# Performance work log

Measured on AMD Instinct MI355X. Metric: run time of the kernel, lower is better.

## Reference

```python
import jax, jax.numpy as jnp
import numpy as np

N_NODES = 250000
N_EDGES = 4000000
N_GRAPHS = 512
NEG_SLOPE = 0.01  # F.leaky_relu default


def _glorot(key, shape):
    fan_in, fan_out = shape
    lim = (6.0 / (fan_in + fan_out)) ** 0.5
    return jax.random.uniform(key, shape, jnp.float32, -lim, lim)


def setup_inputs() -> dict:
    key = jax.random.key(0)
    ks = jax.random.split(key, 12)
    x = jax.random.normal(ks[0], (N_NODES, 13), jnp.float32)
    edge_index = jax.random.randint(ks[1], (2, N_EDGES), 0, N_NODES, jnp.int64)
    batch_index = jnp.sort(jax.random.randint(ks[2], (N_NODES,), 0, N_GRAPHS, jnp.int64))
    # SAGEConv params: lin_l (neighbor agg, with bias), lin_r (self, no bias)
    dims = [(13, 16), (16, 8), (8, 4)]
    params = {}
    for i, (di, do) in enumerate(dims, 1):
        params[f'W{i}l'] = _glorot(ks[2 + 2 * i], (di, do))
        params[f'b{i}'] = jnp.zeros((do,), jnp.float32)
        params[f'W{i}r'] = _glorot(ks[3 + 2 * i], (di, do))
    params['Wc'] = _glorot(ks[10], (8, 1))
    params['bc'] = jnp.zeros((1,), jnp.float32)
    return dict(x=x, edge_index=edge_index, batch_index=batch_index, **params)


def _sage_conv(x, src, dst, Wl, bl, Wr):
    # mean-aggregate neighbor features at target nodes, then linear
    msg_sum = jax.ops.segment_sum(x[src], dst, num_segments=N_NODES)  # [N, d]
    cnt = jax.ops.segment_sum(jnp.ones((src.shape[0],), x.dtype), dst,
                              num_segments=N_NODES)
    agg = msg_sum / jnp.maximum(cnt, 1.0)[:, None]
    return agg @ Wl + bl + x @ Wr


def reference(x, edge_index, batch_index,
              W1l, b1, W1r, W2l, b2, W2r, W3l, b3, W3r, Wc, bc):
    src, dst = edge_index[0], edge_index[1]
    h = jax.nn.leaky_relu(_sage_conv(x, src, dst, W1l, b1, W1r), NEG_SLOPE)
    h = jax.nn.leaky_relu(_sage_conv(h, src, dst, W2l, b2, W2r), NEG_SLOPE)
    h = _sage_conv(h, src, dst, W3l, b3, W3r)  # [N, 4]
    add_pool = jax.ops.segment_sum(h, batch_index, num_segments=N_GRAPHS)  # [G,4]
    gcnt = jax.ops.segment_sum(jnp.ones((N_NODES,), h.dtype), batch_index,
                               num_segments=N_GRAPHS)
    mean_pool = add_pool / jnp.maximum(gcnt, 1.0)[:, None]
    g = jnp.concatenate([mean_pool, add_pool], axis=1)  # [G, 8]
    return g @ Wc + bc  # [G, 1]
```

## Files before the change

### kernel.cpp

```cpp
#include <hip/hip_runtime.h>

#define N_NODES 250000
#define N_EDGES 4000000
#define N_GRAPHS 512
#define NEG 0.01f
#define BINB 9
#define WIN 512
#define NBINS 489
#define NSUB (NBINS * 4)
#define CAPQ 2560
#define PART_EPB 8192
#define PART_BLOCKS 489

__device__ __forceinline__ float lrelu(float v) { return v > 0.0f ? v : NEG * v; }
__device__ __forceinline__ unsigned f2b(float f) {
    unsigned u = __float_as_uint(f);
    unsigned r = ((u >> 16) & 1u) + 0x7FFFu;
    return (u + r) >> 16;
}
__device__ __forceinline__ unsigned pk(float a, float b) { return f2b(a) | (f2b(b) << 16); }
__device__ __forceinline__ float blo(unsigned p) { return __uint_as_float(p << 16); }
__device__ __forceinline__ float bhi(unsigned p) { return __uint_as_float(p & 0xFFFF0000u); }

__global__ void pack_x(const float* __restrict__ x, unsigned* __restrict__ x16b,
                       int* __restrict__ qcnt) {
    if (blockIdx.x == 0) {
        for (int i = threadIdx.x; i < NSUB; i += 256) qcnt[i] = 0;
    }
    int tid = blockIdx.x * blockDim.x + threadIdx.x;
    if (tid >= N_NODES * 8) return;
    int n = tid >> 3, d2 = tid & 7;
    int a = d2 * 2, b = a + 1;
    float va = (a < 13) ? x[n * 13 + a] : 0.0f;
    float vb = (b < 13) ? x[n * 13 + b] : 0.0f;
    x16b[tid] = pk(va, vb);
}

__global__ __launch_bounds__(1024) void partition_k(const int* __restrict__ src,
                                                    const int* __restrict__ dst,
                                                    int* __restrict__ qcnt,
                                                    unsigned* __restrict__ binned) {
    __shared__ int hist[NSUB];
    __shared__ int base[NSUB];
    int t = threadIdx.x;
    for (int i = t; i < NSUB; i += 1024) hist[i] = 0;
    __syncthreads();
    unsigned e0 = blockIdx.x * PART_EPB;
    for (int i = 0; i < PART_EPB / 1024; i++) {
        unsigned e = e0 + (unsigned)i * 1024u + t;
        if (e < N_EDGES) {
            int s = ((dst[e] >> BINB) << 2) | (src[e] >> 16);
            atomicAdd(&hist[s], 1);
        }
    }
    __syncthreads();
    for (int i = t; i < NSUB; i += 1024) {
        int h = hist[i];
        base[i] = (h > 0) ? atomicAdd(&qcnt[i], h) : 0;
        hist[i] = 0;
    }
    __syncthreads();
    for (int i = 0; i < PART_EPB / 1024; i++) {
        unsigned e = e0 + (unsigned)i * 1024u + t;
        if (e < N_EDGES) {
            int d = dst[e], sv = src[e];
            int s = ((d >> BINB) << 2) | (sv >> 16);
            int pos = base[s] + atomicAdd(&hist[s], 1);
            binned[(size_t)s * CAPQ + pos] =
                ((unsigned)(d & (WIN - 1)) << 18) | (unsigned)sv;
        }
    }
}

__global__ __launch_bounds__(1024) void sortagg_k(const unsigned* __restrict__ x16b,
                                                  unsigned* __restrict__ binned,
                                                  const int* __restrict__ qcnt,
                                                  int* __restrict__ offs,
                                                  float* __restrict__ cntf,
                                                  float* __restrict__ agg) {
    __shared__ unsigned stg[CAPQ];
    __shared__ unsigned srt[CAPQ];
    __shared__ int hist[WIN];
    __shared__ int cur[WIN];
    __shared__ int wsum[8];
    int t = threadIdx.x;
    int bin = blockIdx.x;
    int f = t & (WIN - 1), l = t >> 9;
    int lane = t & 63, wv = t >> 6;
    float a0 = 0, a1 = 0, a2 = 0, a3 = 0, a4 = 0, a5 = 0, a6 = 0, a7 = 0;
    int deg = 0;
    for (int q = 0; q < 4; q++) {
        int sub = (bin << 2) | q;
        int cnt = qcnt[sub];
        unsigned* bp = binned + (size_t)sub * CAPQ;
        if (t < WIN) hist[t] = 0;
        __syncthreads();
        for (int i = t; i < cnt; i += 1024) {
            unsigned w = bp[i];
            stg[i] = w;
            atomicAdd(&hist[w >> 18], 1);
        }
        __syncthreads();
        int v = (t < WIN) ? hist[t] : 0;
#pragma unroll
        for (int d = 1; d < 64; d <<= 1) {
            int u = __shfl_up(v, d, 64);
            if (lane >= d) v += u;
        }
        if (t < WIN && lane == 63) wsum[wv] = v;
        __syncthreads();
        if (t == 0) {
            int r = 0;
#pragma unroll
            for (int i = 0; i < 8; i++) { int s = wsum[i]; wsum[i] = r; r += s; }
        }
        __syncthreads();
        if (t < WIN) {
            int incl = v + wsum[wv];
            int ex = incl - hist[t];
            cur[t] = ex;
            offs[(size_t)sub * 513 + t] = ex;
            deg += hist[t];
        }
        if (t == 0) offs[(size_t)sub * 513 + WIN] = cnt;
        __syncthreads();
        for (int i = t; i < cnt; i += 1024) {
            unsigned w = stg[i];
            int pos = atomicAdd(&cur[w >> 18], 1);
            srt[pos] = w;
        }
        __syncthreads();
        for (int i = t; i < cnt; i += 1024) bp[i] = srt[i];
        int e_ = cur[f];
        int s_ = e_ - hist[f];
        int k = s_;
        for (; k + 4 <= e_; k += 4) {
            unsigned w0 = srt[k], w1 = srt[k + 1], w2 = srt[k + 2], w3 = srt[k + 3];
            uint4 v0 = *(const uint4*)&x16b[(size_t)(w0 & 0x3FFFFu) * 8u + (unsigned)(l * 4)];
            uint4 v1 = *(const uint4*)&x16b[(size_t)(w1 & 0x3FFFFu) * 8u + (unsigned)(l * 4)];
            uint4 v2 = *(const uint4*)&x16b[(size_t)(w2 & 0x3FFFFu) * 8u + (unsigned)(l * 4)];
            uint4 v3 = *(const uint4*)&x16b[(size_t)(w3 & 0x3FFFFu) * 8u + (unsigned)(l * 4)];
            a0 += blo(v0.x) + blo(v1.x) + blo(v2.x) + blo(v3.x);
            a1 += bhi(v0.x) + bhi(v1.x) + bhi(v2.x) + bhi(v3.x);
            a2 += blo(v0.y) + blo(v1.y) + blo(v2.y) + blo(v3.y);
            a3 += bhi(v0.y) + bhi(v1.y) + bhi(v2.y) + bhi(v3.y);
            a4 += blo(v0.z) + blo(v1.z) + blo(v2.z) + blo(v3.z);
            a5 += bhi(v0.z) + bhi(v1.z) + bhi(v2.z) + bhi(v3.z);
            a6 += blo(v0.w) + blo(v1.w) + blo(v2.w) + blo(v3.w);
            a7 += bhi(v0.w) + bhi(v1.w) + bhi(v2.w) + bhi(v3.w);
        }
        for (; k < e_; k++) {
            unsigned w = srt[k];
            uint4 v4 = *(const uint4*)&x16b[(size_t)(w & 0x3FFFFu) * 8u + (unsigned)(l * 4)];
            a0 += blo(v4.x); a1 += bhi(v4.x); a2 += blo(v4.y); a3 += bhi(v4.y);
            a4 += blo(v4.z); a5 += bhi(v4.z); a6 += blo(v4.w); a7 += bhi(v4.w);
        }
        __syncthreads();
    }
    int g = (bin << BINB) + f;
    if (g < N_NODES) {
        size_t b = (size_t)g * 13;
        if (l == 0) {
            agg[b + 0] = a0; agg[b + 1] = a1; agg[b + 2] = a2; agg[b + 3] = a3;
            agg[b + 4] = a4; agg[b + 5] = a5; agg[b + 6] = a6; agg[b + 7] = a7;
            cntf[g] = (float)deg;
        } else {
            agg[b + 8] = a0; agg[b + 9] = a1; agg[b + 10] = a2;
            agg[b + 11] = a3; agg[b + 12] = a4;
        }
    }
}

__global__ void fused1(const float* __restrict__ agg, const float* __restrict__ x,
                       const float* __restrict__ cntf,
                       const float* __restrict__ W1l, const float* __restrict__ b1,
                       const float* __restrict__ W1r, const float* __restrict__ W2l,
                       const float* __restrict__ W2r,
                       unsigned* __restrict__ y2b, float* __restrict__ z2) {
    __shared__ float sWl[208], sWr[208], sb[16], sA[128], sB[128];
    for (int i = threadIdx.x; i < 208; i += blockDim.x) { sWl[i] = W1l[i]; sWr[i] = W1r[i]; }
    for (int i = threadIdx.x; i < 128; i += blockDim.x) { sA[i] = W2l[i]; sB[i] = W2r[i]; }
    if (threadIdx.x < 16) sb[threadIdx.x] = b1[threadIdx.x];
    __syncthreads();
    int n = blockIdx.x * blockDim.x + threadIdx.x;
    if (n >= N_NODES) return;
    float inv = 1.0f / fmaxf(cntf[n], 1.0f);
    float a[13], xv[13];
#pragma unroll
    for (int i = 0; i < 13; i++) { a[i] = agg[n * 13 + i] * inv; xv[i] = x[n * 13 + i]; }
    float h[16];
#pragma unroll
    for (int o = 0; o < 16; o++) {
        float acc = sb[o];
#pragma unroll
        for (int i = 0; i < 13; i++) acc += a[i] * sWl[i * 16 + o] + xv[i] * sWr[i * 16 + o];
        h[o] = lrelu(acc);
    }
    float ya[8];
#pragma unroll
    for (int o2 = 0; o2 < 8; o2++) {
        float y = 0.0f, za = 0.0f;
#pragma unroll
        for (int o = 0; o < 16; o++) { y += h[o] * sA[o * 8 + o2]; za += h[o] * sB[o * 8 + o2]; }
        ya[o2] = y;
        z2[n * 8 + o2] = za;
    }
    uint4 out;
    out.x = pk(ya[0], ya[1]); out.y = pk(ya[2], ya[3]);
    out.z = pk(ya[4], ya[5]); out.w = pk(ya[6], ya[7]);
    *(uint4*)&y2b[(size_t)n * 4u] = out;
}

__global__ __launch_bounds__(256) void agg8f_k(const unsigned* __restrict__ y2b,
                                               const unsigned* __restrict__ binned,
                                               const int* __restrict__ offs,
                                               const float* __restrict__ cntf,
                                               const float* __restrict__ b2,
                                               const float* __restrict__ W3l,
                                               float* __restrict__ z2h2,
                                               unsigned* __restrict__ y3b,
                                               float* __restrict__ pool) {
    __shared__ float sb[8], sW3[32];
    if (blockIdx.x == 0) {
        for (int i = threadIdx.x; i < N_GRAPHS * 5; i += 256) pool[i] = 0.0f;
    }
    if (threadIdx.x < 8) sb[threadIdx.x] = b2[threadIdx.x];
    if (threadIdx.x < 32) sW3[threadIdx.x] = W3l[threadIdx.x];
    __syncthreads();
    int g = blockIdx.x * 256 + threadIdx.x;
    if (g >= N_NODES) return;
    int bin = g >> BINB, f = g & (WIN - 1);
    float a0 = 0, a1 = 0, a2 = 0, a3 = 0, a4 = 0, a5 = 0, a6 = 0, a7 = 0;
#pragma unroll
    for (int q = 0; q < 4; q++) {
        int sub = (bin << 2) | q;
        const int* o = offs + (size_t)sub * 513;
        int s = o[f], e = o[f + 1];
        const unsigned* bp = binned + (size_t)sub * CAPQ;
        int k = s;
        for (; k + 4 <= e; k += 4) {
            unsigned w0 = bp[k], w1 = bp[k + 1], w2 = bp[k + 2], w3 = bp[k + 3];
            uint4 v0 = *(const uint4*)&y2b[(size_t)(w0 & 0x3FFFFu) * 4u];
            uint4 v1 = *(const uint4*)&y2b[(size_t)(w1 & 0x3FFFFu) * 4u];
            uint4 v2 = *(const uint4*)&y2b[(size_t)(w2 & 0x3FFFFu) * 4u];
            uint4 v3 = *(const uint4*)&y2b[(size_t)(w3 & 0x3FFFFu) * 4u];
            a0 += blo(v0.x) + blo(v1.x) + blo(v2.x) + blo(v3.x);
            a1 += bhi(v0.x) + bhi(v1.x) + bhi(v2.x) + bhi(v3.x);
            a2 += blo(v0.y) + blo(v1.y) + blo(v2.y) + blo(v3.y);
            a3 += bhi(v0.y) + bhi(v1.y) + bhi(v2.y) + bhi(v3.y);
            a4 += blo(v0.z) + blo(v1.z) + blo(v2.z) + blo(v3.z);
            a5 += bhi(v0.z) + bhi(v1.z) + bhi(v2.z) + bhi(v3.z);
            a6 += blo(v0.w) + blo(v1.w) + blo(v2.w) + blo(v3.w);
            a7 += bhi(v0.w) + bhi(v1.w) + bhi(v2.w) + bhi(v3.w);
        }
        for (; k < e; k++) {
            uint4 v = *(const uint4*)&y2b[(size_t)(bp[k] & 0x3FFFFu) * 4u];
            a0 += blo(v.x); a1 += bhi(v.x); a2 += blo(v.y); a3 += bhi(v.y);
            a4 += blo(v.z); a5 += bhi(v.z); a6 += blo(v.w); a7 += bhi(v.w);
        }
    }
    float inv = 1.0f / fmaxf(cntf[g], 1.0f);
    float h2v[8];
    float s8[8] = {a0, a1, a2, a3, a4, a5, a6, a7};
#pragma unroll
    for (int j = 0; j < 8; j++) {
        float v = s8[j] * inv + sb[j] + z2h2[(size_t)g * 8 + j];
        h2v[j] = lrelu(v);
        z2h2[(size_t)g * 8 + j] = h2v[j];
    }
    float y[4];
#pragma unroll
    for (int k = 0; k < 4; k++) {
        float acc = 0.0f;
#pragma unroll
        for (int j = 0; j < 8; j++) acc += h2v[j] * sW3[j * 4 + k];
        y[k] = acc;
    }
    uint2 out;
    out.x = pk(y[0], y[1]); out.y = pk(y[2], y[3]);
    *(uint2*)&y3b[(size_t)g * 2u] = out;
}

__global__ __launch_bounds__(256) void agg4pool_k(const unsigned* __restrict__ y3b,
                                                  const unsigned* __restrict__ binned,
                                                  const int* __restrict__ offs,
                                                  const float* __restrict__ cntf,
                                                  const float* __restrict__ h2,
                                                  const float* __restrict__ W3r,
                                                  const float* __restrict__ b3,
                                                  const int* __restrict__ batch,
                                                  float* __restrict__ pool,
                                                  float* __restrict__ gcnt) {
    __shared__ float sW[32], sb[4];
    __shared__ float lp[16][4];
    __shared__ float lc[16];
    __shared__ int sbase;
    if (threadIdx.x < 32) sW[threadIdx.x] = W3r[threadIdx.x];
    if (threadIdx.x < 4) sb[threadIdx.x] = b3[threadIdx.x];
    if (threadIdx.x < 16) {
        lc[threadIdx.x] = 0.0f;
        for (int k = 0; k < 4; k++) lp[threadIdx.x][k] = 0.0f;
    }
    int n0 = blockIdx.x * 256;
    if (threadIdx.x == 0) sbase = batch[n0 < N_NODES ? n0 : N_NODES - 1];
    __syncthreads();
    int g = n0 + threadIdx.x;
    if (g < N_NODES) {
        int bin = g >> BINB, f = g & (WIN - 1);
        float a0 = 0, a1 = 0, a2 = 0, a3 = 0;
#pragma unroll
        for (int q = 0; q < 4; q++) {
            int sub = (bin << 2) | q;
            const int* o = offs + (size_t)sub * 513;
            int s = o[f], e = o[f + 1];
            const unsigned* bp = binned + (size_t)sub * CAPQ;
            int k = s;
            for (; k + 4 <= e; k += 4) {
                unsigned w0 = bp[k], w1 = bp[k + 1], w2 = bp[k + 2], w3 = bp[k + 3];
                uint2 v0 = *(const uint2*)&y3b[(size_t)(w0 & 0x3FFFFu) * 2u];
                uint2 v1 = *(const uint2*)&y3b[(size_t)(w1 & 0x3FFFFu) * 2u];
                uint2 v2 = *(const uint2*)&y3b[(size_t)(w2 & 0x3FFFFu) * 2u];
                uint2 v3 = *(const uint2*)&y3b[(size_t)(w3 & 0x3FFFFu) * 2u];
                a0 += blo(v0.x) + blo(v1.x) + blo(v2.x) + blo(v3.x);
                a1 += bhi(v0.x) + bhi(v1.x) + bhi(v2.x) + bhi(v3.x);
                a2 += blo(v0.y) + blo(v1.y) + blo(v2.y) + blo(v3.y);
                a3 += bhi(v0.y) + bhi(v1.y) + bhi(v2.y) + bhi(v3.y);
            }
            for (; k < e; k++) {
                uint2 v = *(const uint2*)&y3b[(size_t)(bp[k] & 0x3FFFFu) * 2u];
                a0 += blo(v.x); a1 += bhi(v.x); a2 += blo(v.y); a3 += bhi(v.y);
            }
        }
        float inv = 1.0f / fmaxf(cntf[g], 1.0f);
        float s4[4] = {a0, a1, a2, a3};
        float h2v[8];
#pragma unroll
        for (int j = 0; j < 8; j++) h2v[j] = h2[(size_t)g * 8 + j];
        int b = batch[g];
        int off = b - sbase;
        bool local = (off >= 0 && off < 16);
#pragma unroll
        for (int k = 0; k < 4; k++) {
            float z = 0.0f;
#pragma unroll
            for (int j = 0; j < 8; j++) z += h2v[j] * sW[j * 4 + k];
            float v = s4[k] * inv + sb[k] + z;
            if (local) atomicAdd(&lp[off][k], v);
            else atomicAdd(&pool[b * 4 + k], v);
        }
        if (local) atomicAdd(&lc[off], 1.0f);
        else atomicAdd(&gcnt[b], 1.0f);
    }
    __syncthreads();
    if (threadIdx.x < 16) {
        int b = sbase + threadIdx.x;
        float c = lc[threadIdx.x];
        if (c > 0.0f && b < N_GRAPHS) {
            atomicAdd(&gcnt[b], c);
            for (int k = 0; k < 4; k++) atomicAdd(&pool[b * 4 + k], lp[threadIdx.x][k]);
        }
    }
}

__global__ void final_k(const float* __restrict__ pool, const float* __restrict__ gcnt,
                        const float* __restrict__ Wc, const float* __restrict__ bc,
                        float* __restrict__ out) {
    int g = blockIdx.x * blockDim.x + threadIdx.x;
    if (g >= N_GRAPHS) return;
    float inv = 1.0f / fmaxf(gcnt[g], 1.0f);
    float acc = bc[0];
#pragma unroll
    for (int k = 0; k < 4; k++) {
        float ap = pool[g * 4 + k];
        acc += ap * inv * Wc[k] + ap * Wc[4 + k];
    }
    out[g] = acc;
}

extern "C" void kernel_launch(void* const* d_in, const int* in_sizes, int n_in,
                              void* d_out, int out_size, void* d_ws, size_t ws_size,
                              hipStream_t stream) {
    const float* x = (const float*)d_in[0];
    const int* ei = (const int*)d_in[1];
    const int* src = ei;
    const int* dst = ei + N_EDGES;
    const int* batch = (const int*)d_in[2];
    const float* W1l = (const float*)d_in[3];
    const float* b1 = (const float*)d_in[4];
    const float* W1r = (const float*)d_in[5];
    const float* W2l = (const float*)d_in[6];
    const float* b2 = (const float*)d_in[7];
    const float* W2r = (const float*)d_in[8];
    const float* W3l = (const float*)d_in[9];
    const float* b3 = (const float*)d_in[10];
    const float* W3r = (const float*)d_in[11];
    const float* Wc = (const float*)d_in[12];
    const float* bc = (const float*)d_in[13];
    float* out = (float*)d_out;

    const size_t N = N_NODES;
    unsigned* binned = (unsigned*)d_ws;
    int* qcnt = (int*)(binned + (size_t)NSUB * CAPQ);
    int* offs = qcnt + 2048;
    float* fbase = (float*)(offs + (size_t)NSUB * 513);
    float* agg = fbase;
    float* cntf = fbase + 13 * N;
    float* z2 = cntf + N;
    unsigned* x16b = (unsigned*)(z2 + 8 * N);
    unsigned* y2b = x16b + 8 * N;
    unsigned* y3b = y2b + 4 * N;
    float* pool = (float*)(y3b + 2 * N);
    float* gcnt = pool + N_GRAPHS * 4;

    const int TPB = 256;
    const int NB = (N_NODES + TPB - 1) / TPB;

    pack_x<<<(N_NODES * 8 + TPB - 1) / TPB, TPB, 0, stream>>>(x, x16b, qcnt);
    partition_k<<<PART_BLOCKS, 1024, 0, stream>>>(src, dst, qcnt, binned);
    sortagg_k<<<NBINS, 1024, 0, stream>>>(x16b, binned, qcnt, offs, cntf, agg);
    fused1<<<NB, TPB, 0, stream>>>(agg, x, cntf, W1l, b1, W1r, W2l, W2r, y2b, z2);
    agg8f_k<<<NB, TPB, 0, stream>>>(y2b, binned, offs, cntf, b2, W3l, z2, y3b, pool);
    agg4pool_k<<<NB, TPB, 0, stream>>>(y3b, binned, offs, cntf, z2, W3r, b3, batch, pool, gcnt);
    final_k<<<2, TPB, 0, stream>>>(pool, gcnt, Wc, bc, out);
}
```

Measured before the change: 318.4 us.

## Fuse layer-1 dense transform into sortagg and coalesce partition scatter via LDS

The layer-1 linear, leaky-relu and layer-2 projection (formerly the separate fused1 kernel) now run at the end of sortagg_k, reading the aggregated sums from LDS instead of writing and re-reading a 13-float agg buffer. Self features now come from the packed bf16 x16b instead of the fp32 x. partition_k now computes local prefix offsets and stages edges sorted by sub-bin in LDS before writing, so global writes to binned are contiguous runs. The changes remove a kernel launch and a global round trip and make the scatter writes more coalesced. The cost is more LDS per block (possibly lower occupancy), and the self term is now computed from bf16-rounded x.

```diff
diff --git a/kernel.cpp b/kernel.cpp
--- a/kernel.cpp
+++ b/kernel.cpp
@@ -41,34 +41,63 @@
                                                     int* __restrict__ qcnt,
                                                     unsigned* __restrict__ binned) {
     __shared__ int hist[NSUB];
+    __shared__ int loff[NSUB];
     __shared__ int base[NSUB];
+    __shared__ unsigned ebuf[PART_EPB];
+    __shared__ unsigned short subid[PART_EPB];
+    __shared__ int wsum[16];
     int t = threadIdx.x;
     for (int i = t; i < NSUB; i += 1024) hist[i] = 0;
     __syncthreads();
     unsigned e0 = blockIdx.x * PART_EPB;
-    for (int i = 0; i < PART_EPB / 1024; i++) {
-        unsigned e = e0 + (unsigned)i * 1024u + t;
-        if (e < N_EDGES) {
-            int s = ((dst[e] >> BINB) << 2) | (src[e] >> 16);
-            atomicAdd(&hist[s], 1);
-        }
+    int m = min((int)PART_EPB, (int)(N_EDGES - e0));
+    for (int i = t; i < m; i += 1024) {
+        unsigned e = e0 + i;
+        int s = ((dst[e] >> BINB) << 2) | (src[e] >> 16);
+        atomicAdd(&hist[s], 1);
+    }
+    __syncthreads();
+    int p = 0, s0 = 0, incl = 0;
+    if (t < NSUB / 2) { s0 = hist[2 * t]; p = s0 + hist[2 * t + 1]; }
+    incl = p;
+#pragma unroll
+    for (int d = 1; d < 64; d <<= 1) {
+        int u = __shfl_up(incl, d, 64);
+        if ((t & 63) >= d) incl += u;
+    }
+    if ((t & 63) == 63) wsum[t >> 6] = incl;
+    __syncthreads();
+    if (t == 0) {
+        int r = 0;
+#pragma unroll
+        for (int i = 0; i < 16; i++) { int s = wsum[i]; wsum[i] = r; r += s; }
+    }
+    __syncthreads();
+    if (t < NSUB / 2) {
+        int ex = incl + wsum[t >> 6] - p;
+        loff[2 * t] = ex;
+        loff[2 * t + 1] = ex + s0;
     }
     __syncthreads();
     for (int i = t; i < NSUB; i += 1024) {
         int h = hist[i];
         base[i] = (h > 0) ? atomicAdd(&qcnt[i], h) : 0;
-        hist[i] = 0;
-    }
-    __syncthreads();
-    for (int i = 0; i < PART_EPB / 1024; i++) {
-        unsigned e = e0 + (unsigned)i * 1024u + t;
-        if (e < N_EDGES) {
-            int d = dst[e], sv = src[e];
-            int s = ((d >> BINB) << 2) | (sv >> 16);
-            int pos = base[s] + atomicAdd(&hist[s], 1);
-            binned[(size_t)s * CAPQ + pos] =
-                ((unsigned)(d & (WIN - 1)) << 18) | (unsigned)sv;
-        }
+    }
+    __syncthreads();
+    for (int i = t; i < NSUB; i += 1024) hist[i] = loff[i];
+    __syncthreads();
+    for (int i = t; i < m; i += 1024) {
+        unsigned e = e0 + i;
+        int d = dst[e], sv = src[e];
+        int s = ((d >> BINB) << 2) | (sv >> 16);
+        int pos = atomicAdd(&hist[s], 1);
+        ebuf[pos] = ((unsigned)(d & (WIN - 1)) << 18) | (unsigned)sv;
+        subid[pos] = (unsigned short)s;
+    }
+    __syncthreads();
+    for (int j = t; j < m; j += 1024) {
+        int s = subid[j];
+        binned[(size_t)s * CAPQ + base[s] + (j - loff[s])] = ebuf[j];
     }
 }
 
@@ -77,12 +106,21 @@
                                                   const int* __restrict__ qcnt,
                                                   int* __restrict__ offs,
                                                   float* __restrict__ cntf,
-                                                  float* __restrict__ agg) {
-    __shared__ unsigned stg[CAPQ];
-    __shared__ unsigned srt[CAPQ];
-    __shared__ int hist[WIN];
-    __shared__ int cur[WIN];
-    __shared__ int wsum[8];
+                                                  const float* __restrict__ W1l,
+                                                  const float* __restrict__ b1,
+                                                  const float* __restrict__ W1r,
+                                                  const float* __restrict__ W2l,
+                                                  const float* __restrict__ W2r,
+                                                  unsigned* __restrict__ y2b,
+                                                  float* __restrict__ z2) {
+    __shared__ __align__(16) unsigned char sm[35584];
+    unsigned* stg = (unsigned*)sm;
+    unsigned* srt = stg + CAPQ;
+    int* hist = (int*)(srt + CAPQ);
+    int* cur = hist + WIN;
+    int* wsum = cur + WIN;
+    float* sagg = (float*)sm;
+    float* swt = sagg + 8192;
     int t = threadIdx.x;
     int bin = blockIdx.x;
     int f = t & (WIN - 1), l = t >> 9;
@@ -157,58 +195,64 @@
         }
         __syncthreads();
     }
-    int g = (bin << BINB) + f;
-    if (g < N_NODES) {
-        size_t b = (size_t)g * 13;
-        if (l == 0) {
-            agg[b + 0] = a0; agg[b + 1] = a1; agg[b + 2] = a2; agg[b + 3] = a3;
-            agg[b + 4] = a4; agg[b + 5] = a5; agg[b + 6] = a6; agg[b + 7] = a7;
+    {
+        float av[8] = {a0, a1, a2, a3, a4, a5, a6, a7};
+#pragma unroll
+        for (int i = 0; i < 8; i++) sagg[(f << 4) + (l << 3) + i] = av[i];
+    }
+    for (int i = t; i < 688; i += 1024) {
+        float w;
+        if (i < 208) w = W1l[i];
+        else if (i < 416) w = W1r[i - 208];
+        else if (i < 432) w = b1[i - 416];
+        else if (i < 560) w = W2l[i - 432];
+        else w = W2r[i - 560];
+        swt[i] = w;
+    }
+    __syncthreads();
+    if (t < WIN) {
+        int g = (bin << BINB) + t;
+        if (g < N_NODES) {
+            const float* sWl = swt;
+            const float* sWr = swt + 208;
+            const float* sbb = swt + 416;
+            const float* sA = swt + 432;
+            const float* sB = swt + 560;
+            float inv = 1.0f / (float)max(deg, 1);
+            float a[13], xv[13];
+#pragma unroll
+            for (int i = 0; i < 13; i++) a[i] = sagg[(t << 4) + i] * inv;
+#pragma unroll
+            for (int i2 = 0; i2 < 7; i2++) {
+                unsigned u = x16b[(size_t)g * 8 + i2];
+                xv[2 * i2] = blo(u);
+                if (2 * i2 + 1 < 13) xv[2 * i2 + 1] = bhi(u);
+            }
+            float h[16];
+#pragma unroll
+            for (int o = 0; o < 16; o++) {
+                float acc = sbb[o];
+#pragma unroll
+                for (int i = 0; i < 13; i++) acc += a[i] * sWl[i * 16 + o] + xv[i] * sWr[i * 16 + o];
+                h[o] = lrelu(acc);
+            }
+            float ya[8], z[8];
+#pragma unroll
+            for (int o2 = 0; o2 < 8; o2++) {
+                float y = 0.0f, za = 0.0f;
+#pragma unroll
+                for (int o = 0; o < 16; o++) { y += h[o] * sA[o * 8 + o2]; za += h[o] * sB[o * 8 + o2]; }
+                ya[o2] = y; z[o2] = za;
+            }
+            uint4 o4;
+            o4.x = pk(ya[0], ya[1]); o4.y = pk(ya[2], ya[3]);
+            o4.z = pk(ya[4], ya[5]); o4.w = pk(ya[6], ya[7]);
+            *(uint4*)&y2b[(size_t)g * 4u] = o4;
+            *(float4*)&z2[(size_t)g * 8] = make_float4(z[0], z[1], z[2], z[3]);
+            *(float4*)&z2[(size_t)g * 8 + 4] = make_float4(z[4], z[5], z[6], z[7]);
             cntf[g] = (float)deg;
-        } else {
-            agg[b + 8] = a0; agg[b + 9] = a1; agg[b + 10] = a2;
-            agg[b + 11] = a3; agg[b + 12] = a4;
-        }
-    }
-}
-
-__global__ void fused1(const float* __restrict__ agg, const float* __restrict__ x,
-                       const float* __restrict__ cntf,
-                       const float* __restrict__ W1l, const float* __restrict__ b1,
-                       const float* __restrict__ W1r, const float* __restrict__ W2l,
-                       const float* __restrict__ W2r,
-                       unsigned* __restrict__ y2b, float* __restrict__ z2) {
-    __shared__ float sWl[208], sWr[208], sb[16], sA[128], sB[128];
-    for (int i = threadIdx.x; i < 208; i += blockDim.x) { sWl[i] = W1l[i]; sWr[i] = W1r[i]; }
-    for (int i = threadIdx.x; i < 128; i += blockDim.x) { sA[i] = W2l[i]; sB[i] = W2r[i]; }
-    if (threadIdx.x < 16) sb[threadIdx.x] = b1[threadIdx.x];
-    __syncthreads();
-    int n = blockIdx.x * blockDim.x + threadIdx.x;
-    if (n >= N_NODES) return;
-    float inv = 1.0f / fmaxf(cntf[n], 1.0f);
-    float a[13], xv[13];
-#pragma unroll
-    for (int i = 0; i < 13; i++) { a[i] = agg[n * 13 + i] * inv; xv[i] = x[n * 13 + i]; }
-    float h[16];
-#pragma unroll
-    for (int o = 0; o < 16; o++) {
-        float acc = sb[o];
-#pragma unroll
-        for (int i = 0; i < 13; i++) acc += a[i] * sWl[i * 16 + o] + xv[i] * sWr[i * 16 + o];
-        h[o] = lrelu(acc);
-    }
-    float ya[8];
-#pragma unroll
-    for (int o2 = 0; o2 < 8; o2++) {
-        float y = 0.0f, za = 0.0f;
-#pragma unroll
-        for (int o = 0; o < 16; o++) { y += h[o] * sA[o * 8 + o2]; za += h[o] * sB[o * 8 + o2]; }
-        ya[o2] = y;
-        z2[n * 8 + o2] = za;
-    }
-    uint4 out;
-    out.x = pk(ya[0], ya[1]); out.y = pk(ya[2], ya[3]);
-    out.z = pk(ya[4], ya[5]); out.w = pk(ya[6], ya[7]);
-    *(uint4*)&y2b[(size_t)n * 4u] = out;
+        }
+    }
 }
 
 __global__ __launch_bounds__(256) void agg8f_k(const unsigned* __restrict__ y2b,
@@ -403,8 +447,7 @@
     int* qcnt = (int*)(binned + (size_t)NSUB * CAPQ);
     int* offs = qcnt + 2048;
     float* fbase = (float*)(offs + (size_t)NSUB * 513);
-    float* agg = fbase;
-    float* cntf = fbase + 13 * N;
+    float* cntf = fbase;
     float* z2 = cntf + N;
     unsigned* x16b = (unsigned*)(z2 + 8 * N);
     unsigned* y2b = x16b + 8 * N;
@@ -417,8 +460,8 @@
 
     pack_x<<<(N_NODES * 8 + TPB - 1) / TPB, TPB, 0, stream>>>(x, x16b, qcnt);
     partition_k<<<PART_BLOCKS, 1024, 0, stream>>>(src, dst, qcnt, binned);
-    sortagg_k<<<NBINS, 1024, 0, stream>>>(x16b, binned, qcnt, offs, cntf, agg);
-    fused1<<<NB, TPB, 0, stream>>>(agg, x, cntf, W1l, b1, W1r, W2l, W2r, y2b, z2);
+    sortagg_k<<<NBINS, 1024, 0, stream>>>(x16b, binned, qcnt, offs, cntf,
+                                          W1l, b1, W1r, W2l, W2r, y2b, z2);
     agg8f_k<<<NB, TPB, 0, stream>>>(y2b, binned, offs, cntf, b2, W3l, z2, y3b, pool);
     agg4pool_k<<<NB, TPB, 0, stream>>>(y3b, binned, offs, cntf, z2, W3r, b3, batch, pool, gcnt);
     final_k<<<2, TPB, 0, stream>>>(pool, gcnt, Wc, bc, out);
```

After: 355.0 us. 11.5% more time.

## Stage partitioned edges in shared memory for coalesced bucket writes

Applied to the files above, without the earlier changes.

The partition kernel now computes a block-local exclusive prefix over sub-bin histograms and scatters each edge into a shared-memory buffer ordered by sub-bin. It then writes the buffer out sequentially, so consecutive threads write contiguous runs within each global bucket instead of scattering randomly. This aims to cut uncoalesced global stores. In exchange it uses roughly 60KB of LDS, which lowers occupancy, and adds extra scan and synchronisation steps.

```diff
diff --git a/kernel.cpp b/kernel.cpp
--- a/kernel.cpp
+++ b/kernel.cpp
@@ -41,34 +41,63 @@
                                                     int* __restrict__ qcnt,
                                                     unsigned* __restrict__ binned) {
     __shared__ int hist[NSUB];
+    __shared__ int loff[NSUB];
     __shared__ int base[NSUB];
+    __shared__ unsigned ebuf[PART_EPB];
+    __shared__ unsigned short subid[PART_EPB];
+    __shared__ int wsum[16];
     int t = threadIdx.x;
     for (int i = t; i < NSUB; i += 1024) hist[i] = 0;
     __syncthreads();
     unsigned e0 = blockIdx.x * PART_EPB;
-    for (int i = 0; i < PART_EPB / 1024; i++) {
-        unsigned e = e0 + (unsigned)i * 1024u + t;
-        if (e < N_EDGES) {
-            int s = ((dst[e] >> BINB) << 2) | (src[e] >> 16);
-            atomicAdd(&hist[s], 1);
-        }
+    int m = min((int)PART_EPB, (int)(N_EDGES - e0));
+    for (int i = t; i < m; i += 1024) {
+        unsigned e = e0 + i;
+        int s = ((dst[e] >> BINB) << 2) | (src[e] >> 16);
+        atomicAdd(&hist[s], 1);
+    }
+    __syncthreads();
+    int p = 0, s0 = 0, incl = 0;
+    if (t < NSUB / 2) { s0 = hist[2 * t]; p = s0 + hist[2 * t + 1]; }
+    incl = p;
+#pragma unroll
+    for (int d = 1; d < 64; d <<= 1) {
+        int u = __shfl_up(incl, d, 64);
+        if ((t & 63) >= d) incl += u;
+    }
+    if ((t & 63) == 63) wsum[t >> 6] = incl;
+    __syncthreads();
+    if (t == 0) {
+        int r = 0;
+#pragma unroll
+        for (int i = 0; i < 16; i++) { int s = wsum[i]; wsum[i] = r; r += s; }
+    }
+    __syncthreads();
+    if (t < NSUB / 2) {
+        int ex = incl + wsum[t >> 6] - p;
+        loff[2 * t] = ex;
+        loff[2 * t + 1] = ex + s0;
     }
     __syncthreads();
     for (int i = t; i < NSUB; i += 1024) {
         int h = hist[i];
         base[i] = (h > 0) ? atomicAdd(&qcnt[i], h) : 0;
-        hist[i] = 0;
-    }
-    __syncthreads();
-    for (int i = 0; i < PART_EPB / 1024; i++) {
-        unsigned e = e0 + (unsigned)i * 1024u + t;
-        if (e < N_EDGES) {
-            int d = dst[e], sv = src[e];
-            int s = ((d >> BINB) << 2) | (sv >> 16);
-            int pos = base[s] + atomicAdd(&hist[s], 1);
-            binned[(size_t)s * CAPQ + pos] =
-                ((unsigned)(d & (WIN - 1)) << 18) | (unsigned)sv;
-        }
+    }
+    __syncthreads();
+    for (int i = t; i < NSUB; i += 1024) hist[i] = loff[i];
+    __syncthreads();
+    for (int i = t; i < m; i += 1024) {
+        unsigned e = e0 + i;
+        int d = dst[e], sv = src[e];
+        int s = ((d >> BINB) << 2) | (sv >> 16);
+        int pos = atomicAdd(&hist[s], 1);
+        ebuf[pos] = ((unsigned)(d & (WIN - 1)) << 18) | (unsigned)sv;
+        subid[pos] = (unsigned short)s;
+    }
+    __syncthreads();
+    for (int j = t; j < m; j += 1024) {
+        int s = subid[j];
+        binned[(size_t)s * CAPQ + base[s] + (j - loff[s])] = ebuf[j];
     }
 }
 
```

Measured after the change: 297.2 us. 6.7% less time.
